# Kernel tuning notes

Hardware: AMD Instinct MI355X
Metric: run time of the kernel (lower is better)

## Reference

```python
import jax, jax.numpy as jnp
import numpy as np

Hr, Wr = 64, 2048          # range-view size
Hb, Wb = 512, 512          # BEV size
R_MAX = 50.0
VERT_ROW = Hr // 2         # vert_row default in __init__
B, C = 4, 64
TWO_PI = 2.0 * np.pi


def _sample_coords():
    """Replicates the buffer math in RV2BEV.__init__ + grid_sample's
    align_corners=True unnormalization. Returns flat px (N=Hb*Wb,) and scalar py."""
    yy, xx = np.meshgrid(np.arange(Hb), np.arange(Wb), indexing='ij')
    y = (yy - Hb / 2 + 0.5) * R_MAX / (Hb / 2 - 0.5)
    x = (xx - Wb / 2 + 0.5) * R_MAX / (Wb / 2 - 0.5)
    phi = (np.arctan2(y, x) + TWO_PI) % TWO_PI
    col = Wr - 1 - phi / TWO_PI * (Wr - 1)
    gx = col / Wr * 2 - 1                 # normalized grid x in [-1,1)
    gy = VERT_ROW / Hr * 2 - 1            # normalized grid y (scalar)
    px = (gx + 1) / 2 * (Wr - 1)          # align_corners=True pixel coords
    py = (gy + 1) / 2 * (Hr - 1)
    return px.reshape(-1).astype(np.float32), np.float32(py)

_PX, _PY = _sample_coords()


def _grid_sample_row(rv_feat, px, py):
    """Bilinear grid_sample for a grid whose y-coordinate is a single constant
    row. All coords are in-bounds by construction, so zero-padding never fires."""
    x0 = jnp.floor(px).astype(jnp.int32)
    x1 = jnp.clip(x0 + 1, 0, Wr - 1)
    y0 = int(np.floor(py))
    y1 = min(y0 + 1, Hr - 1)
    wx = (px - x0.astype(px.dtype)).astype(rv_feat.dtype)     # (N,)
    wy = jnp.asarray(py - y0, dtype=rv_feat.dtype)            # scalar
    # interpolate the two relevant RV rows first: (B,C,Wr)
    row = rv_feat[:, :, y0, :] * (1 - wy) + rv_feat[:, :, y1, :] * wy
    # gather along azimuth: (B,C,N)
    s0 = row[:, :, x0]
    s1 = row[:, :, x1]
    return s0 * (1 - wx) + s1 * wx


def setup_inputs() -> dict:
    key = jax.random.key(0)
    k1, k2 = jax.random.split(key)
    rv_feat = jax.random.normal(k1, (B, C, Hr, Wr), dtype=jnp.float32)
    ref_bev = jax.random.normal(k2, (B, C, Hb, Wb), dtype=jnp.float32)
    return {"rv_feat": rv_feat, "ref_bev": ref_bev}


def reference(rv_feat, ref_bev):
    # The torch forward clones ref_bev then overwrites EVERY (b, y, x) index
    # via the scatter (oidx covers all positions of the first B batches), so
    # the result is exactly the sampled features reshaped to the BEV grid.
    sampled = _grid_sample_row(rv_feat, jnp.asarray(_PX), _PY)   # (B,C,N)
    bev = sampled.reshape(rv_feat.shape[0], rv_feat.shape[1], Hb, Wb)
    return bev
```

## Files before the change

### kernel.cpp

```cpp
#include <hip/hip_runtime.h>
#include <math.h>

constexpr int Hr = 64;
constexpr int Wr = 2048;
constexpr int Hb = 512;
constexpr int Wb = 512;
constexpr int B  = 4;
constexpr int C  = 64;
constexpr int BC = B * C;
constexpr int NPIX = Hb * Wb;

constexpr int T = 8192;
constexpr int G = 8;
constexpr int NTILE = NPIX / T;
constexpr int NCG   = BC / G;

typedef float f32x4 __attribute__((ext_vector_type(4)));


__global__ __launch_bounds__(256) void rv2bev_fused(
    const float* __restrict__ rv,
    float* __restrict__ out)
{
    __shared__ float rowbuf[2][Wr];

    const int tile = blockIdx.x;
    const int cg   = blockIdx.y;
    const int tid  = threadIdx.x;

    int   x0[32];
    float wx[32];
    {
        const float cs = 50.0f / 255.5f;
        const float c1 = 2047.0f / 6.28318530717958647692f;
        const float c2 = 2047.0f / 2048.0f;
        #pragma unroll
        for (int k = 0; k < 8; ++k) {
            #pragma unroll
            for (int j = 0; j < 4; ++j) {
                const int n  = tile * T + (tid + k * 256) * 4 + j;
                const float y = ((float)(n >> 9)  - 255.5f) * cs;
                const float x = ((float)(n & 511) - 255.5f) * cs;
                float phi = atan2f(y, x);
                phi = (phi < 0.0f) ? phi + 6.28318530717958647692f : phi;
                const float px = (2047.0f - phi * c1) * c2;
                const float fx = floorf(px);
                x0[k * 4 + j] = (int)fx;
                wx[k * 4 + j] = px - fx;
            }
        }
    }

    const float* rvb = rv + (size_t)(cg * G) * (Hr * Wr) + (size_t)31 * Wr;

    f32x4 sa0, sa1, sb0, sb1;

    {
        const f32x4* r31 = (const f32x4*)rvb;
        const f32x4* r32 = (const f32x4*)(rvb + Wr);
        sa0 = r31[tid]; sa1 = r31[tid + 256];
        sb0 = r32[tid]; sb1 = r32[tid + 256];
        f32x4* dst = (f32x4*)rowbuf[0];
        dst[tid]       = sa0 * 0.5f + sb0 * 0.5f;
        dst[tid + 256] = sa1 * 0.5f + sb1 * 0.5f;
    }

    for (int c = 0; c < G; ++c) {
        if (c + 1 < G) {
            const float* chb = rvb + (size_t)(c + 1) * (Hr * Wr);
            const f32x4* r31 = (const f32x4*)chb;
            const f32x4* r32 = (const f32x4*)(chb + Wr);
            sa0 = r31[tid]; sa1 = r31[tid + 256];
            sb0 = r32[tid]; sb1 = r32[tid + 256];
        }
        __syncthreads();

        const float* __restrict__ row = rowbuf[c & 1];
        f32x4* out4 = (f32x4*)(out + (size_t)(cg * G + c) * NPIX + (size_t)tile * T);
        #pragma unroll
        for (int k = 0; k < 8; ++k) {
            f32x4 r;
            #pragma unroll
            for (int j = 0; j < 4; ++j) {
                const int i = k * 4 + j;
                const float w = wx[i];
                r[j] = row[x0[i]] * (1.0f - w) + row[x0[i] + 1] * w;
            }
            __builtin_nontemporal_store(r, out4 + tid + k * 256);
        }

        if (c + 1 < G) {
            f32x4* dst = (f32x4*)rowbuf[(c + 1) & 1];
            dst[tid]       = sa0 * 0.5f + sb0 * 0.5f;
            dst[tid + 256] = sa1 * 0.5f + sb1 * 0.5f;
        }
    }
}

extern "C" void kernel_launch(void* const* d_in, const int* in_sizes, int n_in,
                              void* d_out, int out_size, void* d_ws, size_t ws_size,
                              hipStream_t stream) {
    const float* rv_feat = (const float*)d_in[0];
    float* out = (float*)d_out;

    rv2bev_fused<<<dim3(NTILE, NCG), dim3(256), 0, stream>>>(rv_feat, out);
}
```

Before: 57.13 us.

## Store adjacent row pairs in LDS and fold angle math into first channel

The shared row buffer now holds (v[i], v[i+1]) pairs, so each bilinear tap costs one 8-byte LDS read instead of two scalar reads. Building the pairs needs one extra global load per half-row for the neighbour element. The per-pixel atan2 setup moves from a separate prologue into the first channel iteration, where it can overlap with that channel's output stores. The kernel also adds a launch-bounds occupancy hint, fully unrolls the channel loop, and replaces floorf with integer truncation, which is valid because the coordinates are positive. The kernel is already dominated by writing a large output, so these savings on LDS traffic and setup may have little effect.

```diff
diff --git a/kernel.cpp b/kernel.cpp
--- a/kernel.cpp
+++ b/kernel.cpp
@@ -16,84 +16,98 @@
 constexpr int NCG   = BC / G;
 
 typedef float f32x4 __attribute__((ext_vector_type(4)));
+typedef float f32x2 __attribute__((ext_vector_type(2)));
 
 
-__global__ __launch_bounds__(256) void rv2bev_fused(
+__global__ __launch_bounds__(256, 4) void rv2bev_fused(
     const float* __restrict__ rv,
     float* __restrict__ out)
 {
-    __shared__ float rowbuf[2][Wr];
+    __shared__ f32x2 buf2[2][Wr];
 
     const int tile = blockIdx.x;
     const int cg   = blockIdx.y;
     const int tid  = threadIdx.x;
 
-    int   x0[32];
-    float wx[32];
-    {
-        const float cs = 50.0f / 255.5f;
-        const float c1 = 2047.0f / 6.28318530717958647692f;
-        const float c2 = 2047.0f / 2048.0f;
-        #pragma unroll
-        for (int k = 0; k < 8; ++k) {
-            #pragma unroll
-            for (int j = 0; j < 4; ++j) {
-                const int n  = tile * T + (tid + k * 256) * 4 + j;
-                const float y = ((float)(n >> 9)  - 255.5f) * cs;
-                const float x = ((float)(n & 511) - 255.5f) * cs;
-                float phi = atan2f(y, x);
-                phi = (phi < 0.0f) ? phi + 6.28318530717958647692f : phi;
-                const float px = (2047.0f - phi * c1) * c2;
-                const float fx = floorf(px);
-                x0[k * 4 + j] = (int)fx;
-                wx[k * 4 + j] = px - fx;
-            }
-        }
-    }
-
     const float* rvb = rv + (size_t)(cg * G) * (Hr * Wr) + (size_t)31 * Wr;
 
+    int   x0t[32];
+    float wxt[32];
+
     f32x4 sa0, sa1, sb0, sb1;
+    float se0, se1, se2, se3;
 
-    {
-        const f32x4* r31 = (const f32x4*)rvb;
-        const f32x4* r32 = (const f32x4*)(rvb + Wr);
-        sa0 = r31[tid]; sa1 = r31[tid + 256];
-        sb0 = r32[tid]; sb1 = r32[tid + 256];
-        f32x4* dst = (f32x4*)rowbuf[0];
-        dst[tid]       = sa0 * 0.5f + sb0 * 0.5f;
-        dst[tid + 256] = sa1 * 0.5f + sb1 * 0.5f;
-    }
+    const int i0 = 4 * tid;
+    const int i1 = 4 * (tid + 256);
 
+    auto issue = [&](int c) {
+        const float* chb = rvb + (size_t)c * (Hr * Wr);
+        const f32x4* r31 = (const f32x4*)chb;
+        const f32x4* r32 = (const f32x4*)(chb + Wr);
+        sa0 = r31[tid];       sa1 = r31[tid + 256];
+        sb0 = r32[tid];       sb1 = r32[tid + 256];
+        se0 = chb[i0 + 4];
+        se1 = chb[Wr + i0 + 4];
+        se2 = chb[i1 + 4];
+        se3 = chb[Wr + i1 + 4];
+    };
+
+    auto writebuf = [&](int nb) {
+        f32x2* d = buf2[nb];
+        const f32x4 a0 = sa0 * 0.5f + sb0 * 0.5f;
+        const f32x4 a1 = sa1 * 0.5f + sb1 * 0.5f;
+        const float n0 = se0 * 0.5f + se1 * 0.5f;
+        const float n1 = se2 * 0.5f + se3 * 0.5f;
+        d[i0 + 0] = f32x2{a0.x, a0.y};
+        d[i0 + 1] = f32x2{a0.y, a0.z};
+        d[i0 + 2] = f32x2{a0.z, a0.w};
+        d[i0 + 3] = f32x2{a0.w, n0};
+        d[i1 + 0] = f32x2{a1.x, a1.y};
+        d[i1 + 1] = f32x2{a1.y, a1.z};
+        d[i1 + 2] = f32x2{a1.z, a1.w};
+        d[i1 + 3] = f32x2{a1.w, n1};
+    };
+
+    issue(0);
+    writebuf(0);
+
+    const float cs = 50.0f / 255.5f;
+    const float c1 = 2047.0f / 6.28318530717958647692f;
+    const float c2 = 2047.0f / 2048.0f;
+
+    #pragma unroll
     for (int c = 0; c < G; ++c) {
-        if (c + 1 < G) {
-            const float* chb = rvb + (size_t)(c + 1) * (Hr * Wr);
-            const f32x4* r31 = (const f32x4*)chb;
-            const f32x4* r32 = (const f32x4*)(chb + Wr);
-            sa0 = r31[tid]; sa1 = r31[tid + 256];
-            sb0 = r32[tid]; sb1 = r32[tid + 256];
-        }
+        if (c + 1 < G) issue(c + 1);
         __syncthreads();
 
-        const float* __restrict__ row = rowbuf[c & 1];
+        const f32x2* __restrict__ rowp = buf2[c & 1];
         f32x4* out4 = (f32x4*)(out + (size_t)(cg * G + c) * NPIX + (size_t)tile * T);
+
         #pragma unroll
         for (int k = 0; k < 8; ++k) {
             f32x4 r;
             #pragma unroll
             for (int j = 0; j < 4; ++j) {
                 const int i = k * 4 + j;
-                const float w = wx[i];
-                r[j] = row[x0[i]] * (1.0f - w) + row[x0[i] + 1] * w;
+                if (c == 0) {
+                    const int n  = tile * T + (tid + k * 256) * 4 + j;
+                    const float y = ((float)(n >> 9)  - 255.5f) * cs;
+                    const float x = ((float)(n & 511) - 255.5f) * cs;
+                    float phi = atan2f(y, x);
+                    phi = (phi < 0.0f) ? phi + 6.28318530717958647692f : phi;
+                    const float px = (2047.0f - phi * c1) * c2;
+                    const int   xi = (int)px;
+                    x0t[i] = xi;
+                    wxt[i] = px - (float)xi;
+                }
+                const float w = wxt[i];
+                const f32x2 v = rowp[x0t[i]];
+                r[j] = v.x * (1.0f - w) + v.y * w;
             }
             __builtin_nontemporal_store(r, out4 + tid + k * 256);
         }
 
-        if (c + 1 < G) {
-            f32x4* dst = (f32x4*)rowbuf[(c + 1) & 1];
-            dst[tid]       = sa0 * 0.5f + sb0 * 0.5f;
-            dst[tid + 256] = sa1 * 0.5f + sb1 * 0.5f;
-        }
+        if (c + 1 < G) writebuf((c + 1) & 1);
     }
 }
 
```

After: 92.72 us. 62.3% more time.

## Precompute sample coordinates in a prep kernel and sample one channel per block

Applied to the files above, without the earlier changes.

Splits the work into two kernels. A prep kernel computes the atan2-based x coordinate for every BEV pixel once and writes it to workspace. The sampling kernel then reads these precomputed coordinates instead of recomputing atan2 in each block, and each block now handles a single channel with a larger pixel tile. The aim is to take the transcendental math off the hot path. In exchange it adds a second launch and extra global reads of the coordinate buffer for every channel, and it drops the cross-channel double-buffered row prefetch.

```diff
diff --git a/kernel.cpp b/kernel.cpp
--- a/kernel.cpp
+++ b/kernel.cpp
@@ -10,90 +10,65 @@
 constexpr int BC = B * C;
 constexpr int NPIX = Hb * Wb;
 
-constexpr int T = 8192;
-constexpr int G = 8;
-constexpr int NTILE = NPIX / T;
-constexpr int NCG   = BC / G;
+constexpr int T   = 16384;
+constexpr int NT  = NPIX / T;
+constexpr int TPB = 128;
 
 typedef float f32x4 __attribute__((ext_vector_type(4)));
 
 
-__global__ __launch_bounds__(256) void rv2bev_fused(
+__global__ __launch_bounds__(256) void prep_px(float* __restrict__ pxbuf)
+{
+    const int n  = blockIdx.x * 256 + threadIdx.x;
+    const float cs = 50.0f / 255.5f;
+    const float c1 = 2047.0f / 6.28318530717958647692f;
+    const float c2 = 2047.0f / 2048.0f;
+    const float y = ((float)(n >> 9)  - 255.5f) * cs;
+    const float x = ((float)(n & 511) - 255.5f) * cs;
+    float phi = atan2f(y, x);
+    phi = (phi < 0.0f) ? phi + 6.28318530717958647692f : phi;
+    pxbuf[n] = (2047.0f - phi * c1) * c2;
+}
+
+__global__ __launch_bounds__(TPB) void sample_kernel(
     const float* __restrict__ rv,
+    const float* __restrict__ pxbuf,
     float* __restrict__ out)
 {
-    __shared__ float rowbuf[2][Wr];
+    __shared__ float row[Wr];
 
     const int tile = blockIdx.x;
-    const int cg   = blockIdx.y;
+    const int ch   = blockIdx.y;
     const int tid  = threadIdx.x;
 
-    int   x0[32];
-    float wx[32];
     {
-        const float cs = 50.0f / 255.5f;
-        const float c1 = 2047.0f / 6.28318530717958647692f;
-        const float c2 = 2047.0f / 2048.0f;
+        const float* chb = rv + (size_t)ch * (Hr * Wr) + (size_t)31 * Wr;
+        const f32x4* r31 = (const f32x4*)chb;
+        const f32x4* r32 = (const f32x4*)(chb + Wr);
+        f32x4* dst = (f32x4*)row;
         #pragma unroll
-        for (int k = 0; k < 8; ++k) {
-            #pragma unroll
-            for (int j = 0; j < 4; ++j) {
-                const int n  = tile * T + (tid + k * 256) * 4 + j;
-                const float y = ((float)(n >> 9)  - 255.5f) * cs;
-                const float x = ((float)(n & 511) - 255.5f) * cs;
-                float phi = atan2f(y, x);
-                phi = (phi < 0.0f) ? phi + 6.28318530717958647692f : phi;
-                const float px = (2047.0f - phi * c1) * c2;
-                const float fx = floorf(px);
-                x0[k * 4 + j] = (int)fx;
-                wx[k * 4 + j] = px - fx;
-            }
+        for (int q = 0; q < 4; ++q) {
+            const int i = tid + q * TPB;
+            dst[i] = r31[i] * 0.5f + r32[i] * 0.5f;
         }
     }
+    __syncthreads();
 
-    const float* rvb = rv + (size_t)(cg * G) * (Hr * Wr) + (size_t)31 * Wr;
+    const f32x4* px4  = (const f32x4*)(pxbuf + (size_t)tile * T);
+    f32x4*       out4 = (f32x4*)(out + (size_t)ch * NPIX + (size_t)tile * T);
 
-    f32x4 sa0, sa1, sb0, sb1;
-
-    {
-        const f32x4* r31 = (const f32x4*)rvb;
-        const f32x4* r32 = (const f32x4*)(rvb + Wr);
-        sa0 = r31[tid]; sa1 = r31[tid + 256];
-        sb0 = r32[tid]; sb1 = r32[tid + 256];
-        f32x4* dst = (f32x4*)rowbuf[0];
-        dst[tid]       = sa0 * 0.5f + sb0 * 0.5f;
-        dst[tid + 256] = sa1 * 0.5f + sb1 * 0.5f;
-    }
-
-    for (int c = 0; c < G; ++c) {
-        if (c + 1 < G) {
-            const float* chb = rvb + (size_t)(c + 1) * (Hr * Wr);
-            const f32x4* r31 = (const f32x4*)chb;
-            const f32x4* r32 = (const f32x4*)(chb + Wr);
-            sa0 = r31[tid]; sa1 = r31[tid + 256];
-            sb0 = r32[tid]; sb1 = r32[tid + 256];
+    #pragma unroll 4
+    for (int k = 0; k < T / 4 / TPB; ++k) {
+        const int i = k * TPB + tid;
+        const f32x4 p = px4[i];
+        f32x4 r;
+        #pragma unroll
+        for (int j = 0; j < 4; ++j) {
+            const int   xi = (int)p[j];
+            const float w  = p[j] - (float)xi;
+            r[j] = row[xi] * (1.0f - w) + row[xi + 1] * w;
         }
-        __syncthreads();
-
-        const float* __restrict__ row = rowbuf[c & 1];
-        f32x4* out4 = (f32x4*)(out + (size_t)(cg * G + c) * NPIX + (size_t)tile * T);
-        #pragma unroll
-        for (int k = 0; k < 8; ++k) {
-            f32x4 r;
-            #pragma unroll
-            for (int j = 0; j < 4; ++j) {
-                const int i = k * 4 + j;
-                const float w = wx[i];
-                r[j] = row[x0[i]] * (1.0f - w) + row[x0[i] + 1] * w;
-            }
-            __builtin_nontemporal_store(r, out4 + tid + k * 256);
-        }
-
-        if (c + 1 < G) {
-            f32x4* dst = (f32x4*)rowbuf[(c + 1) & 1];
-            dst[tid]       = sa0 * 0.5f + sb0 * 0.5f;
-            dst[tid + 256] = sa1 * 0.5f + sb1 * 0.5f;
-        }
+        __builtin_nontemporal_store(r, out4 + i);
     }
 }
 
@@ -102,6 +77,8 @@
                               hipStream_t stream) {
     const float* rv_feat = (const float*)d_in[0];
     float* out = (float*)d_out;
+    float* pxbuf = (float*)d_ws;
 
-    rv2bev_fused<<<dim3(NTILE, NCG), dim3(256), 0, stream>>>(rv_feat, out);
+    prep_px<<<dim3(NPIX / 256), dim3(256), 0, stream>>>(pxbuf);
+    sample_kernel<<<dim3(NT, BC), dim3(TPB), 0, stream>>>(rv_feat, pxbuf, out);
 }
```

Result: slower. 62.85 us (+10.0%).

## Precompute sample indices and weights in a prep kernel instead of per block

Applied to the files above, without the earlier changes.

Moves the atan2-based computation of azimuth indices and interpolation weights out of the main kernel into a separate prep kernel that writes them to workspace once. Before, each of the 32 channel-group blocks per tile recomputed the same 32 atan2 values per thread. The main kernel now loads the precomputed int and float vectors instead. The lerp is also rewritten as a + w*(b-a). The cost is an extra kernel launch plus 2 MB of workspace traffic, and floorf is replaced by truncation, which matches only because px is nonnegative.

```diff
diff --git a/kernel.cpp b/kernel.cpp
--- a/kernel.cpp
+++ b/kernel.cpp
@@ -16,10 +16,38 @@
 constexpr int NCG   = BC / G;
 
 typedef float f32x4 __attribute__((ext_vector_type(4)));
+typedef int   i32x4 __attribute__((ext_vector_type(4)));
 
 
-__global__ __launch_bounds__(256) void rv2bev_fused(
+__global__ __launch_bounds__(256) void prep_px(
+    i32x4* __restrict__ xig,
+    f32x4* __restrict__ wg)
+{
+    const int g  = blockIdx.x * 256 + threadIdx.x;
+    const float cs = 50.0f / 255.5f;
+    const float c1 = 2047.0f / 6.28318530717958647692f;
+    const float c2 = 2047.0f / 2048.0f;
+    i32x4 xo; f32x4 wo;
+    #pragma unroll
+    for (int j = 0; j < 4; ++j) {
+        const int n = g * 4 + j;
+        const float y = ((float)(n >> 9)  - 255.5f) * cs;
+        const float x = ((float)(n & 511) - 255.5f) * cs;
+        float phi = atan2f(y, x);
+        phi = (phi < 0.0f) ? phi + 6.28318530717958647692f : phi;
+        const float px = (2047.0f - phi * c1) * c2;
+        const int   xi = (int)px;
+        xo[j] = xi;
+        wo[j] = px - (float)xi;
+    }
+    xig[g] = xo;
+    wg[g]  = wo;
+}
+
+__global__ __launch_bounds__(256) void rv2bev_main(
     const float* __restrict__ rv,
+    const i32x4* __restrict__ xig,
+    const f32x4* __restrict__ wg,
     float* __restrict__ out)
 {
     __shared__ float rowbuf[2][Wr];
@@ -28,26 +56,18 @@
     const int cg   = blockIdx.y;
     const int tid  = threadIdx.x;
 
-    int   x0[32];
-    float wx[32];
+    int   xi[32];
+    float w[32];
     {
-        const float cs = 50.0f / 255.5f;
-        const float c1 = 2047.0f / 6.28318530717958647692f;
-        const float c2 = 2047.0f / 2048.0f;
+        const i32x4* xs = xig + (size_t)tile * (T / 4);
+        const f32x4* ws = wg  + (size_t)tile * (T / 4);
         #pragma unroll
         for (int k = 0; k < 8; ++k) {
+            const int gidx = tid + k * 256;
+            const i32x4 xv = xs[gidx];
+            const f32x4 wv = ws[gidx];
             #pragma unroll
-            for (int j = 0; j < 4; ++j) {
-                const int n  = tile * T + (tid + k * 256) * 4 + j;
-                const float y = ((float)(n >> 9)  - 255.5f) * cs;
-                const float x = ((float)(n & 511) - 255.5f) * cs;
-                float phi = atan2f(y, x);
-                phi = (phi < 0.0f) ? phi + 6.28318530717958647692f : phi;
-                const float px = (2047.0f - phi * c1) * c2;
-                const float fx = floorf(px);
-                x0[k * 4 + j] = (int)fx;
-                wx[k * 4 + j] = px - fx;
-            }
+            for (int j = 0; j < 4; ++j) { xi[4 * k + j] = xv[j]; w[4 * k + j] = wv[j]; }
         }
     }
 
@@ -77,14 +97,16 @@
 
         const float* __restrict__ row = rowbuf[c & 1];
         f32x4* out4 = (f32x4*)(out + (size_t)(cg * G + c) * NPIX + (size_t)tile * T);
+
         #pragma unroll
         for (int k = 0; k < 8; ++k) {
             f32x4 r;
             #pragma unroll
             for (int j = 0; j < 4; ++j) {
                 const int i = k * 4 + j;
-                const float w = wx[i];
-                r[j] = row[x0[i]] * (1.0f - w) + row[x0[i] + 1] * w;
+                const float a = row[xi[i]];
+                const float b = row[xi[i] + 1];
+                r[j] = a + w[i] * (b - a);
             }
             __builtin_nontemporal_store(r, out4 + tid + k * 256);
         }
@@ -103,5 +125,9 @@
     const float* rv_feat = (const float*)d_in[0];
     float* out = (float*)d_out;
 
-    rv2bev_fused<<<dim3(NTILE, NCG), dim3(256), 0, stream>>>(rv_feat, out);
+    i32x4* xig = (i32x4*)d_ws;
+    f32x4* wg  = (f32x4*)((char*)d_ws + NPIX * 4);
+
+    prep_px<<<dim3(NPIX / 4 / 256), dim3(256), 0, stream>>>(xig, wg);
+    rv2bev_main<<<dim3(NTILE, NCG), dim3(256), 0, stream>>>(rv_feat, xig, wg, out);
 }
```

New measurement: 60.67 us. +6.2%, slower.
